# Performance work log

Measured on AMD Instinct MI355X. Metric: run time of the kernel, lower is better.

The kernel has to match this reference:

```python
import jax, jax.numpy as jnp
import numpy as np

B, N, M, DIM, H, DH = 2, 2048, 2048, 512, 8, 64
INNER = H * DH  # 512


def setup_inputs() -> dict:
    key = jax.random.key(0)
    ks = jax.random.split(key, 9)
    s = 0.02
    return {
        "x": jax.random.normal(ks[0], (B, N, DIM), jnp.float32),
        "x1": jax.random.normal(ks[1], (B, M, DIM), jnp.float32),
        "attn_mat": jax.random.normal(ks[2], (B, H, N, M), jnp.float32),
        "dots_para": jax.random.uniform(ks[3], (1,), jnp.float32),
        "mat_para": jax.random.uniform(ks[4], (1,), jnp.float32),
        "W_qv": jax.random.normal(ks[5], (DIM, 2 * INNER), jnp.float32) * s,
        "W_k": jax.random.normal(ks[6], (DIM, INNER), jnp.float32) * s,
        "W_out": jax.random.normal(ks[7], (INNER, DIM), jnp.float32) * s,
        "b_out": jax.random.normal(ks[8], (DIM,), jnp.float32) * s,
    }


def _split_heads(t):
    # [b, n, h*d] -> [b, h, n, d]
    b, n, _ = t.shape
    return t.reshape(b, n, H, DH).transpose(0, 2, 1, 3)


def reference(x, x1, attn_mat, dots_para, mat_para, W_qv, W_k, W_out, b_out):
    scale = DH ** -0.5
    qv = x @ W_qv                      # [b, n, 2*inner]
    q, v = jnp.split(qv, 2, axis=-1)
    q = _split_heads(q)                # [b, h, n, d]
    v = _split_heads(v)                # [b, h, n, d]
    k = _split_heads(x1 @ W_k)         # [b, h, m, d]
    dots = jnp.einsum("bhnd,bhmd->bhnm", q, k) * scale
    dots = dots * dots_para + attn_mat * mat_para
    attn = jax.nn.softmax(dots, axis=-1)
    out = jnp.einsum("bhnm,bhmd->bhnd", attn, v)
    out = out.transpose(0, 2, 1, 3).reshape(x.shape[0], x.shape[1], INNER)
    return out @ W_out + b_out
```

## Files before the change

### kernel.cpp

```cpp
#include <hip/hip_runtime.h>
#include <hip/hip_bf16.h>

#define NB 2048
#define MB 2048
#define SPLITS 4
#define MSP (MB / SPLITS)

typedef __attribute__((ext_vector_type(8))) short short8;
typedef __attribute__((ext_vector_type(4))) float floatx4;

__device__ __forceinline__ unsigned short f2bf(float f) {
    union { float f; unsigned int u; } v; v.f = f;
    unsigned int r = (v.u + 0x7FFFu + ((v.u >> 16) & 1u)) >> 16;
    return (unsigned short)r;
}

__device__ __forceinline__ int swz(int row, int k) {
    return (row << 6) + ((((k >> 3) ^ (row & 7))) << 3) + (k & 7);
}
__device__ __forceinline__ int vswz(int row, int k) {
    return (row << 6) + ((((k >> 3) ^ (row & 7) ^ ((row >> 3) & 7))) << 3) + (k & 7);
}

__launch_bounds__(256)
__global__ void prep(const float* __restrict__ x, const float* __restrict__ x1,
                     const float* __restrict__ Wqv, const float* __restrict__ Wk,
                     const float* __restrict__ Wout,
                     unsigned short* __restrict__ xb, unsigned short* __restrict__ x1b,
                     unsigned short* __restrict__ Wqvt, unsigned short* __restrict__ Wkt,
                     unsigned short* __restrict__ Woutt) {
    __shared__ float t[64][65];
    const int bid = blockIdx.x, tid = threadIdx.x;
    if (bid < 2048) {
        const float* in = bid < 1024 ? x : x1;
        unsigned short* out = bid < 1024 ? xb : x1b;
        size_t off = ((size_t)(bid & 1023) * 256 + tid) * 8;
        float4 d0 = *(const float4*)(in + off);
        float4 d1 = *(const float4*)(in + off + 4);
        uint4 o;
        o.x = (unsigned int)f2bf(d0.x) | ((unsigned int)f2bf(d0.y) << 16);
        o.y = (unsigned int)f2bf(d0.z) | ((unsigned int)f2bf(d0.w) << 16);
        o.z = (unsigned int)f2bf(d1.x) | ((unsigned int)f2bf(d1.y) << 16);
        o.w = (unsigned int)f2bf(d1.z) | ((unsigned int)f2bf(d1.w) << 16);
        *(uint4*)(out + off) = o;
        return;
    }
    int tb = bid - 2048;
    const float* W; unsigned short* Wt; int N;
    if (tb < 128)      { W = Wqv;  Wt = Wqvt;  N = 1024; }
    else if (tb < 192) { tb -= 128; W = Wk;   Wt = Wkt;   N = 512; }
    else               { tb -= 192; W = Wout; Wt = Woutt; N = 512; }
    const int k0 = (tb & 7) * 64, n0 = (tb >> 3) * 64;
#pragma unroll
    for (int p = 0; p < 4; p++) {
        int idx = p * 256 + tid;
        int kr = idx >> 4, c4 = (idx & 15) << 2;
        float4 d = *(const float4*)(W + (size_t)(k0 + kr) * N + n0 + c4);
        t[kr][c4 + 0] = d.x; t[kr][c4 + 1] = d.y; t[kr][c4 + 2] = d.z; t[kr][c4 + 3] = d.w;
    }
    __syncthreads();
#pragma unroll
    for (int p = 0; p < 4; p++) {
        int idx = p * 256 + tid;
        int nr = idx >> 4, k4 = (idx & 15) << 2;
        uint2 o;
        o.x = (unsigned int)f2bf(t[k4 + 0][nr]) | ((unsigned int)f2bf(t[k4 + 1][nr]) << 16);
        o.y = (unsigned int)f2bf(t[k4 + 2][nr]) | ((unsigned int)f2bf(t[k4 + 3][nr]) << 16);
        *(uint2*)(Wt + (size_t)(n0 + nr) * 512 + k0 + k4) = o;
    }
}

template <int OUT_BF16>
__device__ __forceinline__ void gemm64_body(const unsigned short* __restrict__ A,
                                            const unsigned short* __restrict__ Bt,
                                            const float* __restrict__ bias,
                                            void* __restrict__ Cp, int Nc, int m0, int n0,
                                            short* Al, short* Bl) {
    const int tid = threadIdx.x;
    const int w = tid >> 6, lane = tid & 63;
    const int quad = lane >> 4, c16 = lane & 15;
    const int wr = (w >> 1) * 32, wc = (w & 1) * 32;

    floatx4 acc[2][2];
#pragma unroll
    for (int i = 0; i < 2; i++)
#pragma unroll
        for (int j = 0; j < 2; j++) acc[i][j] = floatx4{0.f, 0.f, 0.f, 0.f};

    for (int kk = 0; kk < 512; kk += 64) {
        __syncthreads();
#pragma unroll
        for (int p = 0; p < 2; p++) {
            int id = p * 256 + tid;
            int row = id >> 3, c8 = (id & 7) << 3;
            *(uint4*)&Al[swz(row, c8)] = *(const uint4*)(A + (size_t)(m0 + row) * 512 + kk + c8);
            *(uint4*)&Bl[swz(row, c8)] = *(const uint4*)(Bt + (size_t)(n0 + row) * 512 + kk + c8);
        }
        __syncthreads();
#pragma unroll
        for (int kc = 0; kc < 2; kc++) {
            short8 af[2], bf[2];
#pragma unroll
            for (int mt = 0; mt < 2; mt++)
                af[mt] = *(const short8*)&Al[swz(wr + mt * 16 + c16, kc * 32 + quad * 8)];
#pragma unroll
            for (int nt = 0; nt < 2; nt++)
                bf[nt] = *(const short8*)&Bl[swz(wc + nt * 16 + c16, kc * 32 + quad * 8)];
#pragma unroll
            for (int mt = 0; mt < 2; mt++)
#pragma unroll
                for (int nt = 0; nt < 2; nt++)
                    acc[mt][nt] = __builtin_amdgcn_mfma_f32_16x16x32_bf16(af[mt], bf[nt], acc[mt][nt], 0, 0, 0);
        }
    }
#pragma unroll
    for (int mt = 0; mt < 2; mt++)
#pragma unroll
        for (int nt = 0; nt < 2; nt++)
#pragma unroll
            for (int r = 0; r < 4; r++) {
                int row = m0 + wr + mt * 16 + quad * 4 + r;
                int col = n0 + wc + nt * 16 + c16;
                float v = acc[mt][nt][r];
                if (OUT_BF16) {
                    ((unsigned short*)Cp)[(size_t)row * Nc + col] = f2bf(v);
                } else {
                    ((float*)Cp)[(size_t)row * Nc + col] = v + bias[col];
                }
            }
}

__launch_bounds__(256)
__global__ void gemm_qvk(const unsigned short* __restrict__ xb, const unsigned short* __restrict__ x1b,
                         const unsigned short* __restrict__ Wqvt, const unsigned short* __restrict__ Wkt,
                         unsigned short* __restrict__ qvbf, unsigned short* __restrict__ kbf) {
    __shared__ short Al[64 * 64];
    __shared__ short Bl[64 * 64];
    int bid = blockIdx.x;
    if (bid < 1024) {
        gemm64_body<1>(xb, Wqvt, nullptr, qvbf, 1024, (bid & 63) * 64, (bid >> 6) * 64, Al, Bl);
    } else {
        bid -= 1024;
        gemm64_body<1>(x1b, Wkt, nullptr, kbf, 512, (bid & 63) * 64, (bid >> 6) * 64, Al, Bl);
    }
}

__launch_bounds__(256)
__global__ void gemm_out(const unsigned short* __restrict__ A, const unsigned short* __restrict__ Bt,
                         const float* __restrict__ bias, float* __restrict__ C) {
    __shared__ short Al[64 * 64];
    __shared__ short Bl[64 * 64];
    gemm64_body<0>(A, Bt, bias, C, 512, blockIdx.x * 64, blockIdx.y * 64, Al, Bl);
}

__launch_bounds__(256)
__global__ void flash_attn(const unsigned short* __restrict__ qv,
                           const unsigned short* __restrict__ kb,
                           const float* __restrict__ attn_mat,
                           const float* __restrict__ dots_para,
                           const float* __restrict__ mat_para,
                           float* __restrict__ Opart,
                           float* __restrict__ lpart) {
    __shared__ short QP[4][32 * 64];
    __shared__ short Ks[2][64 * 64];
    __shared__ short Vs[2][64 * 64];

    const int tid = threadIdx.x, w = tid >> 6, lane = tid & 63;
    const int quad = lane >> 4, c16 = lane & 15;
    const int q0 = blockIdx.x * 128;
    const int bh = blockIdx.y;
    const int sp = blockIdx.z;
    const int b = bh >> 3, h = bh & 7;
    const int ms = sp * MSP;

    const float log2e = 1.4426950408889634f;
    const float mp = mat_para[0] * log2e;
    const float sdp = dots_para[0] * 0.125f * log2e;

    short* QPf = (short*)QP;
#pragma unroll
    for (int p = 0; p < 4; p++) {
        int id = p * 256 + tid;
        int r = id >> 3, c = id & 7;
        *(uint4*)&QPf[swz(r, c * 8)] =
            *(const uint4*)(qv + (size_t)(b * NB + q0 + r) * 1024 + h * 64 + c * 8);
    }
    __syncthreads();
    short8 qf[2][2];
#pragma unroll
    for (int at = 0; at < 2; at++)
#pragma unroll
        for (int kc = 0; kc < 2; kc++)
            qf[at][kc] = *(const short8*)&QPf[swz(w * 32 + at * 16 + c16, kc * 32 + quad * 8)];
    short* Pw = &QPf[w * 2048];

    const int sr = tid >> 3, sc = tid & 7;
    uint4 kreg[2], vreg[2];
    auto loadKV = [&](int m) {
#pragma unroll
        for (int p = 0; p < 2; p++) {
            int r = p * 32 + sr;
            kreg[p] = *(const uint4*)(kb + (size_t)(b * MB + m + r) * 512 + h * 64 + sc * 8);
            vreg[p] = *(const uint4*)(qv + (size_t)(b * NB + m + r) * 1024 + 512 + h * 64 + sc * 8);
        }
    };
    auto storeKV = [&](int bufi) {
#pragma unroll
        for (int p = 0; p < 2; p++) {
            int r = p * 32 + sr;
            *(uint4*)&Ks[bufi][swz(r, sc * 8)] = kreg[p];
            uint4 d = vreg[p];
            Vs[bufi][vswz(sc * 8 + 0, r)] = (short)(d.x & 0xffff);
            Vs[bufi][vswz(sc * 8 + 1, r)] = (short)(d.x >> 16);
            Vs[bufi][vswz(sc * 8 + 2, r)] = (short)(d.y & 0xffff);
            Vs[bufi][vswz(sc * 8 + 3, r)] = (short)(d.y >> 16);
            Vs[bufi][vswz(sc * 8 + 4, r)] = (short)(d.z & 0xffff);
            Vs[bufi][vswz(sc * 8 + 5, r)] = (short)(d.z >> 16);
            Vs[bufi][vswz(sc * 8 + 6, r)] = (short)(d.w & 0xffff);
            Vs[bufi][vswz(sc * 8 + 7, r)] = (short)(d.w >> 16);
        }
    };
    const float* amp = attn_mat + ((size_t)bh * NB + q0 + w * 32 + quad * 4) * MB + c16;
    float amr[2][4][4];
    auto loadAM = [&](int m0_) {
#pragma unroll
        for (int at = 0; at < 2; at++)
#pragma unroll
            for (int r = 0; r < 4; r++)
#pragma unroll
                for (int t = 0; t < 4; t++)
                    amr[at][t][r] = amp[(size_t)(at * 16 + r) * MB + m0_ + t * 16];
    };

    loadKV(ms);
    storeKV(0);
    loadKV(ms + 64 < ms + MSP ? ms + 64 : ms);
    loadAM(ms);

    floatx4 O[2][4];
    float l[2][4];
#pragma unroll
    for (int at = 0; at < 2; at++)
#pragma unroll
        for (int i = 0; i < 4; i++) { O[at][i] = floatx4{0.f, 0.f, 0.f, 0.f}; l[at][i] = 0.f; }

    for (int it = 0; it < MSP / 64; it++) {
        const int m0 = ms + it * 64;
        const int buf = it & 1, nbuf = buf ^ 1;
        __syncthreads();
        storeKV(nbuf);
        int mnn = m0 + 128; if (mnn >= ms + MSP) mnn = ms;
        loadKV(mnn);

        floatx4 S[2][4];
#pragma unroll
        for (int t = 0; t < 4; t++) {
            short8 kf0 = *(const short8*)&Ks[buf][swz(t * 16 + c16, quad * 8)];
            short8 kf1 = *(const short8*)&Ks[buf][swz(t * 16 + c16, 32 + quad * 8)];
#pragma unroll
            for (int at = 0; at < 2; at++) {
                floatx4 s = floatx4{0.f, 0.f, 0.f, 0.f};
                s = __builtin_amdgcn_mfma_f32_16x16x32_bf16(qf[at][0], kf0, s, 0, 0, 0);
                s = __builtin_amdgcn_mfma_f32_16x16x32_bf16(qf[at][1], kf1, s, 0, 0, 0);
                S[at][t] = s;
            }
        }

#pragma unroll
        for (int at = 0; at < 2; at++)
#pragma unroll
            for (int t = 0; t < 4; t++)
#pragma unroll
                for (int r = 0; r < 4; r++) {
                    float p = exp2f(fmaf(S[at][t][r], sdp, amr[at][t][r] * mp));
                    l[at][r] += p;
                    Pw[swz(at * 16 + quad * 4 + r, t * 16 + c16)] = (short)f2bf(p);
                }
        int mnx = m0 + 64; if (mnx >= ms + MSP) mnx = ms;
        loadAM(mnx);
        __threadfence_block();

        short8 pf[2][2];
#pragma unroll
        for (int at = 0; at < 2; at++)
#pragma unroll
            for (int kc = 0; kc < 2; kc++)
                pf[at][kc] = *(const short8*)&Pw[swz(at * 16 + c16, kc * 32 + quad * 8)];
#pragma unroll
        for (int dt = 0; dt < 4; dt++) {
            short8 vf0 = *(const short8*)&Vs[buf][vswz(dt * 16 + c16, quad * 8)];
            short8 vf1 = *(const short8*)&Vs[buf][vswz(dt * 16 + c16, 32 + quad * 8)];
#pragma unroll
            for (int at = 0; at < 2; at++) {
                O[at][dt] = __builtin_amdgcn_mfma_f32_16x16x32_bf16(pf[at][0], vf0, O[at][dt], 0, 0, 0);
                O[at][dt] = __builtin_amdgcn_mfma_f32_16x16x32_bf16(pf[at][1], vf1, O[at][dt], 0, 0, 0);
            }
        }
    }

#pragma unroll
    for (int at = 0; at < 2; at++) {
#pragma unroll
        for (int r = 0; r < 4; r++) {
            float s = l[at][r];
            s += __shfl_xor(s, 1);
            s += __shfl_xor(s, 2);
            s += __shfl_xor(s, 4);
            s += __shfl_xor(s, 8);
            l[at][r] = s;
        }
        if (c16 == 0) {
#pragma unroll
            for (int r = 0; r < 4; r++)
                lpart[(size_t)(sp * 16 + bh) * NB + q0 + w * 32 + at * 16 + quad * 4 + r] = l[at][r];
        }
#pragma unroll
        for (int dt = 0; dt < 4; dt++)
#pragma unroll
            for (int r = 0; r < 4; r++) {
                size_t row = (size_t)sp * 4096 + b * NB + q0 + w * 32 + at * 16 + quad * 4 + r;
                Opart[row * 512 + h * 64 + dt * 16 + c16] = O[at][dt][r];
            }
    }
}

__launch_bounds__(256)
__global__ void combine_splits(const float* __restrict__ Opart, const float* __restrict__ lpart,
                               unsigned short* __restrict__ ao) {
    int idx = blockIdx.x * 256 + threadIdx.x;
    int row = idx >> 7;
    int col = (idx & 127) << 2;
    int b = row >> 11, n = row & 2047, h = col >> 6;
    float ls = 0.f;
    float4 o = {0.f, 0.f, 0.f, 0.f};
#pragma unroll
    for (int sp = 0; sp < SPLITS; sp++) {
        ls += lpart[(size_t)(sp * 16 + b * 8 + h) * NB + n];
        float4 os = *(const float4*)(Opart + ((size_t)sp * 4096 + row) * 512 + col);
        o.x += os.x; o.y += os.y; o.z += os.z; o.w += os.w;
    }
    float rinv = 1.0f / ls;
    uint2 pk;
    pk.x = (unsigned int)f2bf(o.x * rinv) | ((unsigned int)f2bf(o.y * rinv) << 16);
    pk.y = (unsigned int)f2bf(o.z * rinv) | ((unsigned int)f2bf(o.w * rinv) << 16);
    *(uint2*)(ao + (size_t)row * 512 + col) = pk;
}

extern "C" void kernel_launch(void* const* d_in, const int* in_sizes, int n_in,
                              void* d_out, int out_size, void* d_ws, size_t ws_size,
                              hipStream_t stream) {
    const float* x         = (const float*)d_in[0];
    const float* x1        = (const float*)d_in[1];
    const float* attn_mat  = (const float*)d_in[2];
    const float* dots_para = (const float*)d_in[3];
    const float* mat_para  = (const float*)d_in[4];
    const float* W_qv      = (const float*)d_in[5];
    const float* W_k       = (const float*)d_in[6];
    const float* W_out     = (const float*)d_in[7];
    const float* b_out     = (const float*)d_in[8];
    float* out = (float*)d_out;

    unsigned short* xb    = (unsigned short*)d_ws;
    unsigned short* x1b   = xb    + (size_t)4096 * 512;
    unsigned short* qvbf  = x1b   + (size_t)4096 * 512;
    unsigned short* kbf   = qvbf  + (size_t)4096 * 1024;
    unsigned short* aobf  = kbf   + (size_t)4096 * 512;
    unsigned short* Wqvt  = aobf  + (size_t)4096 * 512;
    unsigned short* Wkt   = Wqvt  + (size_t)1024 * 512;
    unsigned short* Woutt = Wkt   + (size_t)512 * 512;
    float*          Opart = (float*)(Woutt + (size_t)512 * 512);
    float*          lpart = Opart + (size_t)SPLITS * 4096 * 512;

    dim3 blk(256);
    prep<<<2304, blk, 0, stream>>>(x, x1, W_qv, W_k, W_out, xb, x1b, Wqvt, Wkt, Woutt);
    gemm_qvk<<<1536, blk, 0, stream>>>(xb, x1b, Wqvt, Wkt, qvbf, kbf);
    flash_attn<<<dim3(16, 16, SPLITS), blk, 0, stream>>>(qvbf, kbf, attn_mat, dots_para, mat_para, Opart, lpart);
    combine_splits<<<2048, blk, 0, stream>>>(Opart, lpart, aobf);
    gemm_out<<<dim3(64, 8), blk, 0, stream>>>(aobf, Woutt, b_out, out);
}
```

Before: 449.4 us.

## Use 128x128 GEMM tiles with direct-to-LDS loads and tune attention inner loop

GEMM kernels switch from 64x64 to 128x128 tiles per block and load operands straight into LDS via global_load_lds, without XOR swizzling. The attention loop raises wave priority around MFMA sections and converts probabilities to bf16 with a packed hardware instruction. The goal is better operand reuse in the projections and less ALU work in softmax. Larger tiles shrink the grids below the CU count, and the unswizzled LDS layout may cause bank conflicts.

```diff
diff --git a/kernel.cpp b/kernel.cpp
--- a/kernel.cpp
+++ b/kernel.cpp
@@ -1,5 +1,4 @@
 #include <hip/hip_runtime.h>
-#include <hip/hip_bf16.h>
 
 #define NB 2048
 #define MB 2048
@@ -20,6 +19,12 @@
 }
 __device__ __forceinline__ int vswz(int row, int k) {
     return (row << 6) + ((((k >> 3) ^ (row & 7) ^ ((row >> 3) & 7))) << 3) + (k & 7);
+}
+
+__device__ __forceinline__ void gload16(const unsigned short* g, short* l) {
+    __builtin_amdgcn_global_load_lds(
+        (const __attribute__((address_space(1))) void*)g,
+        (__attribute__((address_space(3))) void*)l, 16, 0, 0);
 }
 
 __launch_bounds__(256)
@@ -71,52 +76,55 @@
 }
 
 template <int OUT_BF16>
-__device__ __forceinline__ void gemm64_body(const unsigned short* __restrict__ A,
-                                            const unsigned short* __restrict__ Bt,
-                                            const float* __restrict__ bias,
-                                            void* __restrict__ Cp, int Nc, int m0, int n0,
-                                            short* Al, short* Bl) {
+__device__ __forceinline__ void gemm128_body(const unsigned short* __restrict__ A,
+                                             const unsigned short* __restrict__ Bt,
+                                             const float* __restrict__ bias,
+                                             void* __restrict__ Cp, int Nc, int m0, int n0,
+                                             short* Al, short* Bl) {
     const int tid = threadIdx.x;
     const int w = tid >> 6, lane = tid & 63;
     const int quad = lane >> 4, c16 = lane & 15;
-    const int wr = (w >> 1) * 32, wc = (w & 1) * 32;
-
-    floatx4 acc[2][2];
-#pragma unroll
-    for (int i = 0; i < 2; i++)
-#pragma unroll
-        for (int j = 0; j < 2; j++) acc[i][j] = floatx4{0.f, 0.f, 0.f, 0.f};
+    const int wr = (w >> 1) * 64, wc = (w & 1) * 64;
+
+    floatx4 acc[4][4];
+#pragma unroll
+    for (int i = 0; i < 4; i++)
+#pragma unroll
+        for (int j = 0; j < 4; j++) acc[i][j] = floatx4{0.f, 0.f, 0.f, 0.f};
+
+    const unsigned short* Ap = A + (size_t)m0 * 512;
+    const unsigned short* Bp = Bt + (size_t)n0 * 512;
 
     for (int kk = 0; kk < 512; kk += 64) {
+#pragma unroll
+        for (int p = 0; p < 4; p++) {
+            int idx = p * 256 + tid;
+            int row = idx >> 3, c8 = (idx & 7) << 3;
+            gload16(Ap + (size_t)row * 512 + kk + c8, Al + idx * 8);
+            gload16(Bp + (size_t)row * 512 + kk + c8, Bl + idx * 8);
+        }
         __syncthreads();
 #pragma unroll
-        for (int p = 0; p < 2; p++) {
-            int id = p * 256 + tid;
-            int row = id >> 3, c8 = (id & 7) << 3;
-            *(uint4*)&Al[swz(row, c8)] = *(const uint4*)(A + (size_t)(m0 + row) * 512 + kk + c8);
-            *(uint4*)&Bl[swz(row, c8)] = *(const uint4*)(Bt + (size_t)(n0 + row) * 512 + kk + c8);
+        for (int kc = 0; kc < 2; kc++) {
+            short8 af[4], bf[4];
+#pragma unroll
+            for (int mt = 0; mt < 4; mt++)
+                af[mt] = *(const short8*)&Al[(wr + mt * 16 + c16) * 64 + kc * 32 + quad * 8];
+#pragma unroll
+            for (int nt = 0; nt < 4; nt++)
+                bf[nt] = *(const short8*)&Bl[(wc + nt * 16 + c16) * 64 + kc * 32 + quad * 8];
+#pragma unroll
+            for (int mt = 0; mt < 4; mt++)
+#pragma unroll
+                for (int nt = 0; nt < 4; nt++)
+                    acc[mt][nt] = __builtin_amdgcn_mfma_f32_16x16x32_bf16(af[mt], bf[nt], acc[mt][nt], 0, 0, 0);
         }
         __syncthreads();
-#pragma unroll
-        for (int kc = 0; kc < 2; kc++) {
-            short8 af[2], bf[2];
-#pragma unroll
-            for (int mt = 0; mt < 2; mt++)
-                af[mt] = *(const short8*)&Al[swz(wr + mt * 16 + c16, kc * 32 + quad * 8)];
-#pragma unroll
-            for (int nt = 0; nt < 2; nt++)
-                bf[nt] = *(const short8*)&Bl[swz(wc + nt * 16 + c16, kc * 32 + quad * 8)];
-#pragma unroll
-            for (int mt = 0; mt < 2; mt++)
-#pragma unroll
-                for (int nt = 0; nt < 2; nt++)
-                    acc[mt][nt] = __builtin_amdgcn_mfma_f32_16x16x32_bf16(af[mt], bf[nt], acc[mt][nt], 0, 0, 0);
-        }
-    }
-#pragma unroll
-    for (int mt = 0; mt < 2; mt++)
-#pragma unroll
-        for (int nt = 0; nt < 2; nt++)
+    }
+#pragma unroll
+    for (int mt = 0; mt < 4; mt++)
+#pragma unroll
+        for (int nt = 0; nt < 4; nt++)
 #pragma unroll
             for (int r = 0; r < 4; r++) {
                 int row = m0 + wr + mt * 16 + quad * 4 + r;
@@ -134,23 +142,23 @@
 __global__ void gemm_qvk(const unsigned short* __restrict__ xb, const unsigned short* __restrict__ x1b,
                          const unsigned short* __restrict__ Wqvt, const unsigned short* __restrict__ Wkt,
                          unsigned short* __restrict__ qvbf, unsigned short* __restrict__ kbf) {
-    __shared__ short Al[64 * 64];
-    __shared__ short Bl[64 * 64];
+    __shared__ short Al[128 * 64];
+    __shared__ short Bl[128 * 64];
     int bid = blockIdx.x;
-    if (bid < 1024) {
-        gemm64_body<1>(xb, Wqvt, nullptr, qvbf, 1024, (bid & 63) * 64, (bid >> 6) * 64, Al, Bl);
+    if (bid < 256) {
+        gemm128_body<1>(xb, Wqvt, nullptr, qvbf, 1024, (bid & 31) * 128, (bid >> 5) * 128, Al, Bl);
     } else {
-        bid -= 1024;
-        gemm64_body<1>(x1b, Wkt, nullptr, kbf, 512, (bid & 63) * 64, (bid >> 6) * 64, Al, Bl);
+        bid -= 256;
+        gemm128_body<1>(x1b, Wkt, nullptr, kbf, 512, (bid & 31) * 128, (bid >> 5) * 128, Al, Bl);
     }
 }
 
 __launch_bounds__(256)
 __global__ void gemm_out(const unsigned short* __restrict__ A, const unsigned short* __restrict__ Bt,
                          const float* __restrict__ bias, float* __restrict__ C) {
-    __shared__ short Al[64 * 64];
-    __shared__ short Bl[64 * 64];
-    gemm64_body<0>(A, Bt, bias, C, 512, blockIdx.x * 64, blockIdx.y * 64, Al, Bl);
+    __shared__ short Al[128 * 64];
+    __shared__ short Bl[128 * 64];
+    gemm128_body<0>(A, Bt, bias, C, 512, blockIdx.x * 128, blockIdx.y * 128, Al, Bl);
 }
 
 __launch_bounds__(256)
@@ -253,6 +261,7 @@
         loadKV(mnn);
 
         floatx4 S[2][4];
+        __builtin_amdgcn_s_setprio(1);
 #pragma unroll
         for (int t = 0; t < 4; t++) {
             short8 kf0 = *(const short8*)&Ks[buf][swz(t * 16 + c16, quad * 8)];
@@ -265,17 +274,26 @@
                 S[at][t] = s;
             }
         }
+        __builtin_amdgcn_s_setprio(0);
 
 #pragma unroll
         for (int at = 0; at < 2; at++)
 #pragma unroll
-            for (int t = 0; t < 4; t++)
-#pragma unroll
-                for (int r = 0; r < 4; r++) {
-                    float p = exp2f(fmaf(S[at][t][r], sdp, amr[at][t][r] * mp));
-                    l[at][r] += p;
-                    Pw[swz(at * 16 + quad * 4 + r, t * 16 + c16)] = (short)f2bf(p);
-                }
+            for (int t = 0; t < 4; t++) {
+                float p0 = exp2f(fmaf(S[at][t][0], sdp, amr[at][t][0] * mp));
+                float p1 = exp2f(fmaf(S[at][t][1], sdp, amr[at][t][1] * mp));
+                float p2 = exp2f(fmaf(S[at][t][2], sdp, amr[at][t][2] * mp));
+                float p3 = exp2f(fmaf(S[at][t][3], sdp, amr[at][t][3] * mp));
+                l[at][0] += p0; l[at][1] += p1; l[at][2] += p2; l[at][3] += p3;
+                unsigned int w01, w23;
+                asm("v_cvt_pk_bf16_f32 %0, %1, %2" : "=v"(w01) : "v"(p0), "v"(p1));
+                asm("v_cvt_pk_bf16_f32 %0, %1, %2" : "=v"(w23) : "v"(p2), "v"(p3));
+                int br = at * 16 + quad * 4;
+                Pw[swz(br + 0, t * 16 + c16)] = (short)(w01 & 0xffff);
+                Pw[swz(br + 1, t * 16 + c16)] = (short)(w01 >> 16);
+                Pw[swz(br + 2, t * 16 + c16)] = (short)(w23 & 0xffff);
+                Pw[swz(br + 3, t * 16 + c16)] = (short)(w23 >> 16);
+            }
         int mnx = m0 + 64; if (mnx >= ms + MSP) mnx = ms;
         loadAM(mnx);
         __threadfence_block();
@@ -286,6 +304,7 @@
 #pragma unroll
             for (int kc = 0; kc < 2; kc++)
                 pf[at][kc] = *(const short8*)&Pw[swz(at * 16 + c16, kc * 32 + quad * 8)];
+        __builtin_amdgcn_s_setprio(1);
 #pragma unroll
         for (int dt = 0; dt < 4; dt++) {
             short8 vf0 = *(const short8*)&Vs[buf][vswz(dt * 16 + c16, quad * 8)];
@@ -296,6 +315,7 @@
                 O[at][dt] = __builtin_amdgcn_mfma_f32_16x16x32_bf16(pf[at][1], vf1, O[at][dt], 0, 0, 0);
             }
         }
+        __builtin_amdgcn_s_setprio(0);
     }
 
 #pragma unroll
@@ -373,8 +393,8 @@
 
     dim3 blk(256);
     prep<<<2304, blk, 0, stream>>>(x, x1, W_qv, W_k, W_out, xb, x1b, Wqvt, Wkt, Woutt);
-    gemm_qvk<<<1536, blk, 0, stream>>>(xb, x1b, Wqvt, Wkt, qvbf, kbf);
+    gemm_qvk<<<384, blk, 0, stream>>>(xb, x1b, Wqvt, Wkt, qvbf, kbf);
     flash_attn<<<dim3(16, 16, SPLITS), blk, 0, stream>>>(qvbf, kbf, attn_mat, dots_para, mat_para, Opart, lpart);
     combine_splits<<<2048, blk, 0, stream>>>(Opart, lpart, aobf);
-    gemm_out<<<dim3(64, 8), blk, 0, stream>>>(aobf, Woutt, b_out, out);
-}
+    gemm_out<<<dim3(32, 4), blk, 0, stream>>>(aobf, Woutt, b_out, out);
+}
```

New measurement: 439.3 us. 1.02x faster.
